# Kernel optimization log

Measured on AMD Instinct MI355X. Metric: run time of the kernel, lower is better.

## Reference

```python
import jax, jax.numpy as jnp
import numpy as np
from jax.scipy.special import logsumexp

B, DK, N, M = 16, 512, 1024, 1024
SINKHORN_ITERS = 5
EPS = 1e-8


def setup_inputs() -> dict:
    key = jax.random.key(0)
    k1, k2, k3, k4, k5 = jax.random.split(key, 5)
    return {
        "src_embedding": jax.random.normal(k1, (B, DK, N), dtype=jnp.float32),
        "tgt_embedding": jax.random.normal(k2, (B, DK, M), dtype=jnp.float32),
        "src": jax.random.normal(k3, (B, 3, N), dtype=jnp.float32),
        "tgt": jax.random.normal(k4, (B, 3, M), dtype=jnp.float32),
        # temperature must be positive; uniform in [0.05, 1.0)
        "temperature": jax.random.uniform(k5, (B,), dtype=jnp.float32, minval=0.05, maxval=1.0),
    }


def sinkhorn(scores, n_iters):
    # ZeroPad2d((0,1,0,1)): pad one slack row and one slack column with zeros
    scores = jnp.pad(scores, ((0, 0), (0, 1), (0, 1)))
    for _ in range(n_iters):
        # row normalization (all rows except slack row)
        top = scores[:, :-1, :] - logsumexp(scores[:, :-1, :], axis=2, keepdims=True)
        scores = jnp.concatenate([top, scores[:, -1:, :]], axis=1)
        # column normalization (all cols except slack col)
        left = scores[:, :, :-1] - logsumexp(scores[:, :, :-1], axis=1, keepdims=True)
        scores = jnp.concatenate([left, scores[:, :, -1:]], axis=2)
    return scores[:, :-1, :-1]


def reference(src_embedding, tgt_embedding, src, tgt, temperature):
    b, d_k, n = src_embedding.shape
    # [B, N, M] similarity scores
    dists = jnp.einsum('bdn,bdm->bnm', src_embedding, tgt_embedding) / jnp.sqrt(jnp.float32(d_k))
    affinity = dists / temperature[:, None, None]
    log_perm = sinkhorn(affinity, SINKHORN_ITERS)
    perm = jnp.exp(log_perm)                                             # [B,N,M]
    perm_norm = perm / (jnp.sum(perm, axis=2, keepdims=True) + EPS)      # [B,N,M]
    # soft correspondence: weighted_tgt[b,:,i] = sum_j perm_norm[b,i,j] * tgt[b,:,j]
    weighted_tgt = jnp.einsum('bdm,bnm->bdn', tgt, perm_norm)            # [B,3,N]
    weights = jnp.sum(perm, axis=-1, keepdims=True)                      # [B,N,1]
    weights_norm = weights / (jnp.sum(weights, axis=1, keepdims=True) + EPS)
    weights_norm = jnp.swapaxes(weights_norm, 1, 2)                      # [B,1,N]
    src_centroid = jnp.sum(src * weights_norm, axis=2, keepdims=True)    # [B,3,1]
    tgt_centroid = jnp.sum(weighted_tgt * weights_norm, axis=2, keepdims=True)
    src_centered = src - src_centroid
    corr_centered = (weighted_tgt - tgt_centroid) * weights_norm
    # weighted cross-covariance, batched 3x3
    H = jnp.einsum('bin,bjn->bij', src_centered, corr_centered)          # [B,3,3]
    # batched Procrustes via SVD (torch.svd: H = u diag(s) v^T; jnp: H = u diag(s) vh)
    u, s, vh = jnp.linalg.svd(H)
    v = jnp.swapaxes(vh, 1, 2)
    ut = jnp.swapaxes(u, 1, 2)
    r = jnp.matmul(v, ut)
    r_det = jnp.linalg.det(r)                                            # [B]
    diag = jnp.stack([jnp.ones_like(r_det), jnp.ones_like(r_det), r_det], axis=-1)  # [B,3]
    R = jnp.matmul(v * diag[:, None, :], ut)                             # [B,3,3]
    t = (jnp.matmul(-R, src_centroid) + tgt_centroid).reshape(b, 3)
    return R, t, perm_norm
```

## Files before the change

### kernel.cpp

```cpp
#include <hip/hip_runtime.h>
#include <math.h>

#define BB 16
#define NN 1024
#define MM 1024
#define DKK 512
#define RBLK 16
#define NRB  (NN/RBLK)

typedef short short8 __attribute__((ext_vector_type(8)));
typedef float f32x4 __attribute__((ext_vector_type(4)));

__device__ float g_u[BB*NN];
__device__ float g_v[BB*MM];
__device__ float g_w[BB*NN];
__device__ float g_wt[BB*3*NN];
__device__ float g_pm[BB*NRB*MM];
__device__ float g_ps[BB*NRB*MM];
__device__ __attribute__((aligned(16))) unsigned short gAh[BB*NN*DKK];
__device__ __attribute__((aligned(16))) unsigned short gAl[BB*NN*DKK];
__device__ __attribute__((aligned(16))) unsigned short gBh[BB*MM*DKK];
__device__ __attribute__((aligned(16))) unsigned short gBl[BB*MM*DKK];

__global__ __launch_bounds__(256) void zero_v_kernel() {
    int i = blockIdx.x*256 + threadIdx.x;
    if (i < BB*MM) g_v[i] = 0.0f;
}

__device__ __forceinline__ unsigned int bf16_rne(float x){
    unsigned int u = __float_as_uint(x);
    return (u + 0x7fffu + ((u>>16)&1u)) >> 16;
}

__device__ __forceinline__ void gl_lds(const void* g, void* l){
    __builtin_amdgcn_global_load_lds(
        (const __attribute__((address_space(1))) unsigned int*)g,
        (__attribute__((address_space(3))) unsigned int*)l, 16, 0, 0);
}

__global__ __launch_bounds__(256) void convert_split(const float* __restrict__ A,
                                                     const float* __restrict__ Bm) {
    int z = blockIdx.z;
    int which = z >> 4;
    int b = z & 15;
    const float* X = which ? Bm : A;
    unsigned short* Hh = which ? gBh : gAh;
    unsigned short* Hl = which ? gBl : gAl;
    int d0 = blockIdx.y * 64;
    int i0 = blockIdx.x * 64;
    __shared__ float T[64*65];
    const float* Xb = X + ((size_t)b*DKK + d0)*NN + i0;
    int t = threadIdx.x;
#pragma unroll
    for (int it=0; it<4; ++it){
        int lin = t + 256*it;
        int d = lin >> 4;
        int i4 = lin & 15;
        float4 v = *(const float4*)(Xb + (size_t)d*NN + i4*4);
        T[(i4*4+0)*65 + d] = v.x;
        T[(i4*4+1)*65 + d] = v.y;
        T[(i4*4+2)*65 + d] = v.z;
        T[(i4*4+3)*65 + d] = v.w;
    }
    __syncthreads();
    size_t obase = ((size_t)b*NN + i0)*DKK + d0;
#pragma unroll
    for (int it=0; it<2; ++it){
        int c = t + 256*it;
        int i = c >> 3;
        int p = c & 7;
        unsigned int hw[4], lw[4];
#pragma unroll
        for (int j=0;j<4;j++){
            float x0 = T[i*65 + p*8 + 2*j];
            float x1 = T[i*65 + p*8 + 2*j+1];
            unsigned int h0 = bf16_rne(x0);
            unsigned int h1 = bf16_rne(x1);
            float hf0 = __uint_as_float(h0<<16);
            float hf1 = __uint_as_float(h1<<16);
            unsigned int l0 = bf16_rne(x0 - hf0);
            unsigned int l1 = bf16_rne(x1 - hf1);
            hw[j] = h0 | (h1<<16);
            lw[j] = l0 | (l1<<16);
        }
        int pw = (p & 4) | ((p + (i>>1)) & 3);
        size_t eo = obase + (size_t)i*DKK + pw*8;
        uint4 hv; hv.x=hw[0]; hv.y=hw[1]; hv.z=hw[2]; hv.w=hw[3];
        uint4 lv; lv.x=lw[0]; lv.y=lw[1]; lv.z=lw[2]; lv.w=lw[3];
        *(uint4*)(Hh + eo) = hv;
        *(uint4*)(Hl + eo) = lv;
    }
}

__global__ __launch_bounds__(512,2) void gemm_mfma(const float* __restrict__ temp,
                                                   float* __restrict__ C) {
    int id   = blockIdx.x;
    int xcd  = id & 7;
    int slot = id >> 3;
    int b    = xcd*2 + (slot >> 4);
    int sub  = slot & 15;
    int i0   = (sub >> 2) << 8;
    int j0   = (sub & 3) << 8;
    __shared__ __attribute__((aligned(16))) char lds[131072];
    int t = threadIdx.x;
    int lane = t & 63, w = t >> 6;
    int wr = w >> 2, wc = w & 3;

    int rql = lane >> 2, cl = lane & 3;
    unsigned eoff = (unsigned)(b * (NN*DKK*2));
    unsigned offA = eoff + (unsigned)((i0 + w*32 + rql)*1024) + (unsigned)(cl*16);
    unsigned offB = eoff + (unsigned)((j0 + w*32 + rql)*1024) + (unsigned)(cl*16);
    int dq0 = w*2048;

    const char* pAh = (const char*)gAh;
    const char* pAl = (const char*)gAl;
    const char* pBh = (const char*)gBh;
    const char* pBl = (const char*)gBl;

    f32x4 acc[32];
#pragma unroll
    for (int q=0;q<32;q++) acc[q] = (f32x4){0.f,0.f,0.f,0.f};

    int fslot = ((lane>>4) + ((lane&15)>>1)) & 3;
    int faoff = (wr*128 + (lane&15))*64 + fslot*16;
    int fboff = (wc*64  + (lane&15))*64 + fslot*16;

    gl_lds(pAh + offA,          lds + 0      + dq0);
    gl_lds(pAh + offA + 16384,  lds + 0      + dq0 + 1024);
    gl_lds(pBh + offB,          lds + 65536  + dq0);
    gl_lds(pBh + offB + 16384,  lds + 65536  + dq0 + 1024);
    gl_lds(pAl + offA,          lds + 32768  + dq0);
    gl_lds(pAl + offA + 16384,  lds + 32768  + dq0 + 1024);
    gl_lds(pBl + offB,          lds + 98304  + dq0);
    gl_lds(pBl + offB + 16384,  lds + 98304  + dq0 + 1024);

    short8 ah[8], bh[4], al[8], bl[4];

    for (int ks=0; ks<16; ++ks){
        int par = (ks & 1) << 14;
        int nxt = 16384 - par;

        asm volatile("s_waitcnt vmcnt(4)" ::: "memory");
        __builtin_amdgcn_s_barrier();
        __builtin_amdgcn_sched_barrier(0);
        {
            const char* fa = lds + par + faoff;
            const char* fb = lds + 65536 + par + fboff;
#pragma unroll
            for (int mf=0;mf<8;mf++) ah[mf] = *(const short8*)(fa + mf*1024);
#pragma unroll
            for (int nf=0;nf<4;nf++) bh[nf] = *(const short8*)(fb + nf*1024);
        }
        if (ks < 15){
            offA += 64; offB += 64;
            gl_lds(pAh + offA,         lds + 0     + nxt + dq0);
            gl_lds(pAh + offA + 16384, lds + 0     + nxt + dq0 + 1024);
            gl_lds(pBh + offB,         lds + 65536 + nxt + dq0);
            gl_lds(pBh + offB + 16384, lds + 65536 + nxt + dq0 + 1024);
        }
        asm volatile("s_waitcnt lgkmcnt(0)" ::: "memory");
        __builtin_amdgcn_sched_barrier(0);
        __builtin_amdgcn_s_setprio(1);
#pragma unroll
        for (int nf=0;nf<4;nf++)
#pragma unroll
            for (int mf=0;mf<8;mf++)
                acc[mf*4+nf] = __builtin_amdgcn_mfma_f32_16x16x32_bf16(ah[mf], bh[nf], acc[mf*4+nf], 0,0,0);
        __builtin_amdgcn_s_setprio(0);
        __builtin_amdgcn_sched_barrier(0);

        if (ks < 15) asm volatile("s_waitcnt vmcnt(6)" ::: "memory");
        else         asm volatile("s_waitcnt vmcnt(2)" ::: "memory");
        __builtin_amdgcn_s_barrier();
        __builtin_amdgcn_sched_barrier(0);
        {
            const char* fa = lds + 32768 + par + faoff;
#pragma unroll
            for (int mf=0;mf<8;mf++) al[mf] = *(const short8*)(fa + mf*1024);
        }
        if (ks < 15){
            gl_lds(pAl + offA,         lds + 32768 + nxt + dq0);
            gl_lds(pAl + offA + 16384, lds + 32768 + nxt + dq0 + 1024);
        }
        asm volatile("s_waitcnt lgkmcnt(0)" ::: "memory");
        __builtin_amdgcn_sched_barrier(0);
        __builtin_amdgcn_s_setprio(1);
#pragma unroll
        for (int nf=0;nf<4;nf++)
#pragma unroll
            for (int mf=0;mf<8;mf++)
                acc[mf*4+nf] = __builtin_amdgcn_mfma_f32_16x16x32_bf16(al[mf], bh[nf], acc[mf*4+nf], 0,0,0);
        __builtin_amdgcn_s_setprio(0);
        __builtin_amdgcn_sched_barrier(0);

        if (ks < 15) asm volatile("s_waitcnt vmcnt(6)" ::: "memory");
        else         asm volatile("s_waitcnt vmcnt(0)" ::: "memory");
        __builtin_amdgcn_s_barrier();
        __builtin_amdgcn_sched_barrier(0);
        {
            const char* fb = lds + 98304 + par + fboff;
#pragma unroll
            for (int nf=0;nf<4;nf++) bl[nf] = *(const short8*)(fb + nf*1024);
        }
        if (ks < 15){
            gl_lds(pBl + offB,         lds + 98304 + nxt + dq0);
            gl_lds(pBl + offB + 16384, lds + 98304 + nxt + dq0 + 1024);
        }
        asm volatile("s_waitcnt lgkmcnt(0)" ::: "memory");
        __builtin_amdgcn_sched_barrier(0);
        __builtin_amdgcn_s_setprio(1);
#pragma unroll
        for (int nf=0;nf<4;nf++)
#pragma unroll
            for (int mf=0;mf<8;mf++)
                acc[mf*4+nf] = __builtin_amdgcn_mfma_f32_16x16x32_bf16(ah[mf], bl[nf], acc[mf*4+nf], 0,0,0);
        __builtin_amdgcn_s_setprio(0);
        __builtin_amdgcn_sched_barrier(0);
    }

    float scale = 1.0f/(22.62741699796952f * temp[b]);
    float* Cb = C + ((size_t)b<<20);
    int r0c = i0 + wr*128 + ((lane>>4)<<2);
    int c0c = j0 + wc*64 + (lane&15);
#pragma unroll
    for (int mf=0;mf<8;mf++){
#pragma unroll
        for (int r2=0;r2<4;r2++){
            float* rowp = Cb + (size_t)(r0c + mf*16 + r2)*MM + c0c;
#pragma unroll
            for (int nf=0;nf<4;nf++)
                rowp[nf*16] = acc[mf*4+nf][r2]*scale;
        }
    }
}

__global__ __launch_bounds__(256) void sink_iter(const float* __restrict__ S) {
    int b   = blockIdx.y;
    int rb  = blockIdx.x;
    int row0 = rb*RBLK;
    int t = threadIdx.x;
    __shared__ float Ls[RBLK*1028];
    __shared__ float v_l[1024];
    __shared__ float u_l[RBLK];

    float4 v4 = *(const float4*)(g_v + (b<<10) + t*4);
    *(float4*)(v_l + t*4) = v4;

    const float* Sb = S + ((size_t)b*NN + row0)*MM;
#pragma unroll
    for (int rr=0; rr<RBLK; ++rr){
        float4 s4 = *(const float4*)(Sb + (size_t)rr*MM + t*4);
        s4.x -= v4.x; s4.y -= v4.y; s4.z -= v4.z; s4.w -= v4.w;
        *(float4*)(&Ls[rr*1028 + t*4]) = s4;
    }
    __syncthreads();

    {
        int r = t >> 4, c = t & 15;
        const float* Lr = &Ls[r*1028 + c];
        float m = -INFINITY;
#pragma unroll
        for (int k=0;k<64;k++) m = fmaxf(m, Lr[16*k]);
#pragma unroll
        for (int off=1; off<16; off<<=1) m = fmaxf(m, __shfl_xor(m, off));
        m = fmaxf(m, 0.0f);
        float s = 0.0f;
#pragma unroll
        for (int k=0;k<64;k++) s += __expf(Lr[16*k] - m);
#pragma unroll
        for (int off=1; off<16; off<<=1) s += __shfl_xor(s, off);
        s += __expf(-m);
        float u = m + __logf(s);
        if (c==0){ u_l[r] = u; g_u[b*NN + row0 + r] = u; }
    }
    __syncthreads();

    float mm[4], ss[4];
#pragma unroll
    for (int q=0;q<4;q++){ mm[q]=-INFINITY; ss[q]=0.f; }
#pragma unroll
    for (int r=0;r<RBLK;++r){
        float ur = u_l[r];
        const float* Lr = &Ls[r*1028];
#pragma unroll
        for (int q=0;q<4;q++)
            mm[q] = fmaxf(mm[q], Lr[t + 256*q] - ur);
    }
#pragma unroll
    for (int r=0;r<RBLK;++r){
        float ur = u_l[r];
        const float* Lr = &Ls[r*1028];
#pragma unroll
        for (int q=0;q<4;q++)
            ss[q] += __expf(Lr[t + 256*q] - ur - mm[q]);
    }
    size_t pbase = ((size_t)(b*NRB + rb) << 10) + t;
#pragma unroll
    for (int q=0;q<4;q++){
        g_pm[pbase + 256*q] = mm[q] + v_l[t + 256*q];
        g_ps[pbase + 256*q] = ss[q];
    }
}

__global__ __launch_bounds__(256) void col_lse_combine() {
    int idx = blockIdx.x*256 + threadIdx.x;
    int b = idx >> 10; int j = idx & (MM-1);
    size_t base = ((size_t)(b*NRB) << 10) + j;
    float m[4], s[4];
#pragma unroll
    for (int k=0;k<4;k++){ m[k] = -INFINITY; s[k] = 0.0f; }
    for (int c=0;c<NRB;c+=4){
#pragma unroll
        for (int k=0;k<4;k++){
            float om = g_pm[base + ((size_t)(c+k)<<10)];
            float os = g_ps[base + ((size_t)(c+k)<<10)];
            float nm = fmaxf(m[k], om);
            s[k] = s[k]*__expf(m[k]-nm) + os*__expf(om-nm);
            m[k] = nm;
        }
    }
    float M01 = fmaxf(m[0], m[1]);
    float M23 = fmaxf(m[2], m[3]);
    float Mx  = fmaxf(M01, M23);
    float Sx  = s[0]*__expf(m[0]-Mx) + s[1]*__expf(m[1]-Mx)
              + s[2]*__expf(m[2]-Mx) + s[3]*__expf(m[3]-Mx);
    float nm = fmaxf(Mx, 0.0f);
    Sx = Sx*__expf(Mx-nm) + __expf(-nm);
    g_v[idx] = nm + __logf(Sx);
}

__global__ __launch_bounds__(256) void finalize_rows(float* __restrict__ S,
                                                     const float* __restrict__ tgt) {
    int row  = blockIdx.x*4 + (threadIdx.x>>6);
    int lane = threadIdx.x & 63;
    int b = row >> 10;
    int i = row & (NN-1);
    float ui = g_u[row];
    float4* srow = (float4*)(S + (size_t)row*MM);
    const float4* vb = (const float4*)(g_v + (b<<10));
    const float4* t0 = (const float4*)(tgt + (size_t)b*3*MM);
    const float4* t1 = (const float4*)(tgt + (size_t)b*3*MM + MM);
    const float4* t2 = (const float4*)(tgt + (size_t)b*3*MM + 2*MM);
    float p[16];
    float rs=0.f, a0=0.f, a1=0.f, a2=0.f;
#pragma unroll
    for (int k=0;k<4;k++){
        float4 s4 = srow[lane + 64*k];
        float4 v4 = vb[lane + 64*k];
        p[4*k+0] = __expf(s4.x - ui - v4.x);
        p[4*k+1] = __expf(s4.y - ui - v4.y);
        p[4*k+2] = __expf(s4.z - ui - v4.z);
        p[4*k+3] = __expf(s4.w - ui - v4.w);
        rs += p[4*k+0]+p[4*k+1]+p[4*k+2]+p[4*k+3];
        float4 w0 = t0[lane + 64*k];
        float4 w1 = t1[lane + 64*k];
        float4 w2 = t2[lane + 64*k];
        a0 += p[4*k+0]*w0.x + p[4*k+1]*w0.y + p[4*k+2]*w0.z + p[4*k+3]*w0.w;
        a1 += p[4*k+0]*w1.x + p[4*k+1]*w1.y + p[4*k+2]*w1.z + p[4*k+3]*w1.w;
        a2 += p[4*k+0]*w2.x + p[4*k+1]*w2.y + p[4*k+2]*w2.z + p[4*k+3]*w2.w;
    }
    for (int off=32; off; off>>=1){
        rs += __shfl_xor(rs, off);
        a0 += __shfl_xor(a0, off);
        a1 += __shfl_xor(a1, off);
        a2 += __shfl_xor(a2, off);
    }
    float inv = 1.0f/(rs + 1e-8f);
#pragma unroll
    for (int k=0;k<4;k++){
        srow[lane + 64*k] = make_float4(p[4*k+0]*inv, p[4*k+1]*inv, p[4*k+2]*inv, p[4*k+3]*inv);
    }
    if (lane==0){
        g_w[row] = rs;
        g_wt[(b*3+0)*NN + i] = a0*inv;
        g_wt[(b*3+1)*NN + i] = a1*inv;
        g_wt[(b*3+2)*NN + i] = a2*inv;
    }
}

__global__ __launch_bounds__(256) void procrustes(const float* __restrict__ src,
                                                  float* __restrict__ out) {
    int b = blockIdx.x;
    int t = threadIdx.x;
    __shared__ float red[256];
    auto bsum = [&](float v)->float{
        red[t]=v; __syncthreads();
        for (int o=128;o>0;o>>=1){ if(t<o) red[t]+=red[t+o]; __syncthreads(); }
        float r=red[0]; __syncthreads(); return r;
    };
    const float* wrow = g_w + b*NN;
    float pw=0.f;
    for (int i=t;i<NN;i+=256) pw += wrow[i];
    float W = bsum(pw);
    float winv = 1.0f/(W + 1e-8f);
    const float* sb  = src  + (size_t)b*3*NN;
    const float* wtb = g_wt + (size_t)b*3*NN;
    float sc[3], tc[3];
    for (int c=0;c<3;c++){
        float p1=0.f,p2=0.f;
        for (int i=t;i<NN;i+=256){
            float wn = wrow[i]*winv;
            p1 += sb[c*NN+i]*wn;
            p2 += wtb[c*NN+i]*wn;
        }
        sc[c]=bsum(p1);
        tc[c]=bsum(p2);
    }
    float H[9];
    for (int c=0;c<3;c++)
        for (int d=0;d<3;d++){
            float p=0.f;
            for (int i=t;i<NN;i+=256){
                float wn = wrow[i]*winv;
                p += (sb[c*NN+i]-sc[c]) * ((wtb[d*NN+i]-tc[d])*wn);
            }
            H[c*3+d]=bsum(p);
        }
    if (t==0){
        double Hd[3][3];
        for (int r2=0;r2<3;r2++) for (int c2=0;c2<3;c2++) Hd[r2][c2]=H[r2*3+c2];
        double K[3][3];
        for (int i2=0;i2<3;i2++)
            for (int j2=0;j2<3;j2++){
                double acc=0;
                for (int r2=0;r2<3;r2++) acc += Hd[r2][i2]*Hd[r2][j2];
                K[i2][j2]=acc;
            }
        double V[3][3]={{1,0,0},{0,1,0},{0,0,1}};
        const int PQ[3][2]={{0,1},{0,2},{1,2}};
        for (int sweep=0; sweep<30; ++sweep){
            double off = fabs(K[0][1])+fabs(K[0][2])+fabs(K[1][2]);
            if (off < 1e-26) break;
            for (int pi=0; pi<3; ++pi){
                int p = PQ[pi][0], q = PQ[pi][1];
                double apq = K[p][q];
                if (fabs(apq) < 1e-300) continue;
                double tau = (K[q][q]-K[p][p])/(2.0*apq);
                double tt  = (tau>=0.0?1.0:-1.0)/(fabs(tau)+sqrt(1.0+tau*tau));
                double c   = 1.0/sqrt(1.0+tt*tt);
                double s   = tt*c;
                double Kpp=K[p][p], Kqq=K[q][q];
                K[p][p] = Kpp - tt*apq;
                K[q][q] = Kqq + tt*apq;
                K[p][q] = 0.0; K[q][p] = 0.0;
                int r2 = 3-p-q;
                double Krp=K[r2][p], Krq=K[r2][q];
                K[r2][p] = c*Krp - s*Krq; K[p][r2]=K[r2][p];
                K[r2][q] = s*Krp + c*Krq; K[q][r2]=K[r2][q];
                for (int rr=0; rr<3; ++rr){
                    double vp=V[rr][p], vq=V[rr][q];
                    V[rr][p] = c*vp - s*vq;
                    V[rr][q] = s*vp + c*vq;
                }
            }
        }
        double lam[3]={K[0][0],K[1][1],K[2][2]};
        int o0=0,o1=1,o2=2,tmp;
        if (lam[o0]<lam[o1]){tmp=o0;o0=o1;o1=tmp;}
        if (lam[o0]<lam[o2]){tmp=o0;o0=o2;o2=tmp;}
        if (lam[o1]<lam[o2]){tmp=o1;o1=o2;o2=tmp;}
        int ord[3]={o0,o1,o2};
        double Vs[3][3], U[3][3];
        for (int k=0;k<3;k++)
            for (int r2=0;r2<3;r2++) Vs[r2][k]=V[r2][ord[k]];
        for (int k=0;k<3;k++){
            double ux = Hd[0][0]*Vs[0][k] + Hd[0][1]*Vs[1][k] + Hd[0][2]*Vs[2][k];
            double uy = Hd[1][0]*Vs[0][k] + Hd[1][1]*Vs[1][k] + Hd[1][2]*Vs[2][k];
            double uz = Hd[2][0]*Vs[0][k] + Hd[2][1]*Vs[1][k] + Hd[2][2]*Vs[2][k];
            double n = sqrt(ux*ux+uy*uy+uz*uz);
            if (n > 1e-30){ U[0][k]=ux/n; U[1][k]=uy/n; U[2][k]=uz/n; }
            else {
                double cx = U[1][0]*U[2][1]-U[2][0]*U[1][1];
                double cy = U[2][0]*U[0][1]-U[0][0]*U[2][1];
                double cz = U[0][0]*U[1][1]-U[1][0]*U[0][1];
                U[0][k]=cx; U[1][k]=cy; U[2][k]=cz;
            }
        }
        double rm[3][3];
        for (int i2=0;i2<3;i2++)
            for (int j2=0;j2<3;j2++)
                rm[i2][j2] = Vs[i2][0]*U[j2][0] + Vs[i2][1]*U[j2][1] + Vs[i2][2]*U[j2][2];
        double det = rm[0][0]*(rm[1][1]*rm[2][2]-rm[1][2]*rm[2][1])
                   - rm[0][1]*(rm[1][0]*rm[2][2]-rm[1][2]*rm[2][0])
                   + rm[0][2]*(rm[1][0]*rm[2][1]-rm[1][1]*rm[2][0]);
        double R[3][3];
        for (int i2=0;i2<3;i2++)
            for (int j2=0;j2<3;j2++)
                R[i2][j2] = Vs[i2][0]*U[j2][0] + Vs[i2][1]*U[j2][1] + det*Vs[i2][2]*U[j2][2];
        double tv[3];
        for (int i2=0;i2<3;i2++)
            tv[i2] = -(R[i2][0]*sc[0]+R[i2][1]*sc[1]+R[i2][2]*sc[2]) + tc[i2];
        for (int i2=0;i2<3;i2++)
            for (int j2=0;j2<3;j2++)
                out[b*9 + i2*3 + j2] = (float)R[i2][j2];
        for (int i2=0;i2<3;i2++)
            out[144 + b*3 + i2] = (float)tv[i2];
    }
}

extern "C" void kernel_launch(void* const* d_in, const int* in_sizes, int n_in,
                              void* d_out, int out_size, void* d_ws, size_t ws_size,
                              hipStream_t stream) {
    const float* src_emb = (const float*)d_in[0];
    const float* tgt_emb = (const float*)d_in[1];
    const float* src     = (const float*)d_in[2];
    const float* tgt     = (const float*)d_in[3];
    const float* temp    = (const float*)d_in[4];
    float* out = (float*)d_out;
    float* S = out + 192;

    hipLaunchKernelGGL(zero_v_kernel, dim3(64), dim3(256), 0, stream);
    hipLaunchKernelGGL(convert_split, dim3(16,8,32), dim3(256), 0, stream, src_emb, tgt_emb);
    hipLaunchKernelGGL(gemm_mfma, dim3(256), dim3(512), 0, stream, temp, S);
    for (int it=0; it<5; ++it){
        hipLaunchKernelGGL(sink_iter, dim3(NRB,BB), dim3(256), 0, stream, S);
        hipLaunchKernelGGL(col_lse_combine, dim3(64), dim3(256), 0, stream);
    }
    hipLaunchKernelGGL(finalize_rows, dim3(4096), dim3(256), 0, stream, S, tgt);
    hipLaunchKernelGGL(procrustes, dim3(16), dim3(256), 0, stream, src, out);
}
```

Before: 351.9 us.

## Merge GEMM pipeline stages, pad sinkhorn LDS, widen column combine, warp-shuffle procrustes

The bf16-split GEMM main loop now loads the Ah, Bh and Al fragments together behind one barrier and prefetches all of the next step's hi/lo A tiles at once. That drops one barrier and the explicit LDS wait stages per k-step. The sinkhorn row-tile LDS stride changes from 1028 to 1032 floats, which alters the bank mapping. The column log-sum-exp combine runs on 256 blocks of 64 threads with 8 independent accumulators and a tree merge, giving more parallelism and more memory-level parallelism. Procrustes loads its data once into registers and reduces with wave shuffles instead of repeated shared-memory tree reductions. The trade-offs are higher register pressure in the GEMM and a less staggered load/compute overlap.

```diff
diff --git a/kernel.cpp b/kernel.cpp
--- a/kernel.cpp
+++ b/kernel.cpp
@@ -7,6 +7,7 @@
 #define DKK 512
 #define RBLK 16
 #define NRB  (NN/RBLK)
+#define LSTR 1032
 
 typedef short short8 __attribute__((ext_vector_type(8)));
 typedef float f32x4 __attribute__((ext_vector_type(4)));
@@ -140,16 +141,19 @@
         int par = (ks & 1) << 14;
         int nxt = 16384 - par;
 
-        asm volatile("s_waitcnt vmcnt(4)" ::: "memory");
+        asm volatile("s_waitcnt vmcnt(2)" ::: "memory");
         __builtin_amdgcn_s_barrier();
         __builtin_amdgcn_sched_barrier(0);
         {
-            const char* fa = lds + par + faoff;
-            const char* fb = lds + 65536 + par + fboff;
+            const char* fa  = lds + par + faoff;
+            const char* fb  = lds + 65536 + par + fboff;
+            const char* fal = lds + 32768 + par + faoff;
 #pragma unroll
             for (int mf=0;mf<8;mf++) ah[mf] = *(const short8*)(fa + mf*1024);
 #pragma unroll
             for (int nf=0;nf<4;nf++) bh[nf] = *(const short8*)(fb + nf*1024);
+#pragma unroll
+            for (int mf=0;mf<8;mf++) al[mf] = *(const short8*)(fal + mf*1024);
         }
         if (ks < 15){
             offA += 64; offB += 64;
@@ -157,8 +161,9 @@
             gl_lds(pAh + offA + 16384, lds + 0     + nxt + dq0 + 1024);
             gl_lds(pBh + offB,         lds + 65536 + nxt + dq0);
             gl_lds(pBh + offB + 16384, lds + 65536 + nxt + dq0 + 1024);
-        }
-        asm volatile("s_waitcnt lgkmcnt(0)" ::: "memory");
+            gl_lds(pAl + offA,         lds + 32768 + nxt + dq0);
+            gl_lds(pAl + offA + 16384, lds + 32768 + nxt + dq0 + 1024);
+        }
         __builtin_amdgcn_sched_barrier(0);
         __builtin_amdgcn_s_setprio(1);
 #pragma unroll
@@ -166,25 +171,6 @@
 #pragma unroll
             for (int mf=0;mf<8;mf++)
                 acc[mf*4+nf] = __builtin_amdgcn_mfma_f32_16x16x32_bf16(ah[mf], bh[nf], acc[mf*4+nf], 0,0,0);
-        __builtin_amdgcn_s_setprio(0);
-        __builtin_amdgcn_sched_barrier(0);
-
-        if (ks < 15) asm volatile("s_waitcnt vmcnt(6)" ::: "memory");
-        else         asm volatile("s_waitcnt vmcnt(2)" ::: "memory");
-        __builtin_amdgcn_s_barrier();
-        __builtin_amdgcn_sched_barrier(0);
-        {
-            const char* fa = lds + 32768 + par + faoff;
-#pragma unroll
-            for (int mf=0;mf<8;mf++) al[mf] = *(const short8*)(fa + mf*1024);
-        }
-        if (ks < 15){
-            gl_lds(pAl + offA,         lds + 32768 + nxt + dq0);
-            gl_lds(pAl + offA + 16384, lds + 32768 + nxt + dq0 + 1024);
-        }
-        asm volatile("s_waitcnt lgkmcnt(0)" ::: "memory");
-        __builtin_amdgcn_sched_barrier(0);
-        __builtin_amdgcn_s_setprio(1);
 #pragma unroll
         for (int nf=0;nf<4;nf++)
 #pragma unroll
@@ -198,15 +184,14 @@
         __builtin_amdgcn_s_barrier();
         __builtin_amdgcn_sched_barrier(0);
         {
-            const char* fb = lds + 98304 + par + fboff;
-#pragma unroll
-            for (int nf=0;nf<4;nf++) bl[nf] = *(const short8*)(fb + nf*1024);
+            const char* fbl = lds + 98304 + par + fboff;
+#pragma unroll
+            for (int nf=0;nf<4;nf++) bl[nf] = *(const short8*)(fbl + nf*1024);
         }
         if (ks < 15){
             gl_lds(pBl + offB,         lds + 98304 + nxt + dq0);
             gl_lds(pBl + offB + 16384, lds + 98304 + nxt + dq0 + 1024);
         }
-        asm volatile("s_waitcnt lgkmcnt(0)" ::: "memory");
         __builtin_amdgcn_sched_barrier(0);
         __builtin_amdgcn_s_setprio(1);
 #pragma unroll
@@ -239,7 +224,7 @@
     int rb  = blockIdx.x;
     int row0 = rb*RBLK;
     int t = threadIdx.x;
-    __shared__ float Ls[RBLK*1028];
+    __shared__ float Ls[RBLK*LSTR];
     __shared__ float v_l[1024];
     __shared__ float u_l[RBLK];
 
@@ -251,13 +236,13 @@
     for (int rr=0; rr<RBLK; ++rr){
         float4 s4 = *(const float4*)(Sb + (size_t)rr*MM + t*4);
         s4.x -= v4.x; s4.y -= v4.y; s4.z -= v4.z; s4.w -= v4.w;
-        *(float4*)(&Ls[rr*1028 + t*4]) = s4;
+        *(float4*)(&Ls[rr*LSTR + t*4]) = s4;
     }
     __syncthreads();
 
     {
         int r = t >> 4, c = t & 15;
-        const float* Lr = &Ls[r*1028 + c];
+        const float* Lr = &Ls[r*LSTR + c];
         float m = -INFINITY;
 #pragma unroll
         for (int k=0;k<64;k++) m = fmaxf(m, Lr[16*k]);
@@ -281,7 +266,7 @@
 #pragma unroll
     for (int r=0;r<RBLK;++r){
         float ur = u_l[r];
-        const float* Lr = &Ls[r*1028];
+        const float* Lr = &Ls[r*LSTR];
 #pragma unroll
         for (int q=0;q<4;q++)
             mm[q] = fmaxf(mm[q], Lr[t + 256*q] - ur);
@@ -289,7 +274,7 @@
 #pragma unroll
     for (int r=0;r<RBLK;++r){
         float ur = u_l[r];
-        const float* Lr = &Ls[r*1028];
+        const float* Lr = &Ls[r*LSTR];
 #pragma unroll
         for (int q=0;q<4;q++)
             ss[q] += __expf(Lr[t + 256*q] - ur - mm[q]);
@@ -302,16 +287,16 @@
     }
 }
 
-__global__ __launch_bounds__(256) void col_lse_combine() {
-    int idx = blockIdx.x*256 + threadIdx.x;
+__global__ __launch_bounds__(64) void col_lse_combine() {
+    int idx = blockIdx.x*64 + threadIdx.x;
     int b = idx >> 10; int j = idx & (MM-1);
     size_t base = ((size_t)(b*NRB) << 10) + j;
-    float m[4], s[4];
-#pragma unroll
-    for (int k=0;k<4;k++){ m[k] = -INFINITY; s[k] = 0.0f; }
-    for (int c=0;c<NRB;c+=4){
-#pragma unroll
-        for (int k=0;k<4;k++){
+    float m[8], s[8];
+#pragma unroll
+    for (int k=0;k<8;k++){ m[k] = -INFINITY; s[k] = 0.0f; }
+    for (int c=0;c<NRB;c+=8){
+#pragma unroll
+        for (int k=0;k<8;k++){
             float om = g_pm[base + ((size_t)(c+k)<<10)];
             float os = g_ps[base + ((size_t)(c+k)<<10)];
             float nm = fmaxf(m[k], om);
@@ -319,13 +304,17 @@
             m[k] = nm;
         }
     }
-    float M01 = fmaxf(m[0], m[1]);
-    float M23 = fmaxf(m[2], m[3]);
-    float Mx  = fmaxf(M01, M23);
-    float Sx  = s[0]*__expf(m[0]-Mx) + s[1]*__expf(m[1]-Mx)
-              + s[2]*__expf(m[2]-Mx) + s[3]*__expf(m[3]-Mx);
-    float nm = fmaxf(Mx, 0.0f);
-    Sx = Sx*__expf(Mx-nm) + __expf(-nm);
+#pragma unroll
+    for (int st=1; st<8; st<<=1){
+#pragma unroll
+        for (int k=0;k<8;k+=2*st){
+            float nm = fmaxf(m[k], m[k+st]);
+            s[k] = s[k]*__expf(m[k]-nm) + s[k+st]*__expf(m[k+st]-nm);
+            m[k] = nm;
+        }
+    }
+    float nm = fmaxf(m[0], 0.0f);
+    float Sx = s[0]*__expf(m[0]-nm) + __expf(-nm);
     g_v[idx] = nm + __logf(Sx);
 }
 
@@ -382,40 +371,69 @@
                                                   float* __restrict__ out) {
     int b = blockIdx.x;
     int t = threadIdx.x;
-    __shared__ float red[256];
-    auto bsum = [&](float v)->float{
-        red[t]=v; __syncthreads();
-        for (int o=128;o>0;o>>=1){ if(t<o) red[t]+=red[t+o]; __syncthreads(); }
-        float r=red[0]; __syncthreads(); return r;
-    };
+    int lane = t & 63, w = t >> 6;
+    __shared__ float part[4][16];
     const float* wrow = g_w + b*NN;
-    float pw=0.f;
-    for (int i=t;i<NN;i+=256) pw += wrow[i];
-    float W = bsum(pw);
-    float winv = 1.0f/(W + 1e-8f);
     const float* sb  = src  + (size_t)b*3*NN;
     const float* wtb = g_wt + (size_t)b*3*NN;
-    float sc[3], tc[3];
+
+    float wv[4], sv[3][4], tv3[3][4];
+#pragma unroll
+    for (int k=0;k<4;k++){
+        int i = t + 256*k;
+        wv[k] = wrow[i];
+#pragma unroll
+        for (int c=0;c<3;c++){
+            sv[c][k]  = sb[c*NN+i];
+            tv3[c][k] = wtb[c*NN+i];
+        }
+    }
+
+    auto block_reduce = [&](float* v, int nv){
+        for (int jx=0;jx<nv;jx++){
+            float x = v[jx];
+            for (int off=32;off;off>>=1) x += __shfl_xor(x, off);
+            if (lane==0) part[w][jx] = x;
+        }
+        __syncthreads();
+        for (int jx=0;jx<nv;jx++)
+            v[jx] = part[0][jx]+part[1][jx]+part[2][jx]+part[3][jx];
+        __syncthreads();
+    };
+
+    float W = wv[0]+wv[1]+wv[2]+wv[3];
+    block_reduce(&W, 1);
+    float winv = 1.0f/(W + 1e-8f);
+    float wn[4];
+#pragma unroll
+    for (int k=0;k<4;k++) wn[k] = wv[k]*winv;
+
+    float a[6];
+#pragma unroll
     for (int c=0;c<3;c++){
         float p1=0.f,p2=0.f;
-        for (int i=t;i<NN;i+=256){
-            float wn = wrow[i]*winv;
-            p1 += sb[c*NN+i]*wn;
-            p2 += wtb[c*NN+i]*wn;
-        }
-        sc[c]=bsum(p1);
-        tc[c]=bsum(p2);
-    }
+#pragma unroll
+        for (int k=0;k<4;k++){ p1 += sv[c][k]*wn[k]; p2 += tv3[c][k]*wn[k]; }
+        a[c]=p1; a[3+c]=p2;
+    }
+    block_reduce(a, 6);
+    float sc[3], tc[3];
+#pragma unroll
+    for (int c=0;c<3;c++){ sc[c]=a[c]; tc[c]=a[3+c]; }
+
     float H[9];
+#pragma unroll
     for (int c=0;c<3;c++)
+#pragma unroll
         for (int d=0;d<3;d++){
             float p=0.f;
-            for (int i=t;i<NN;i+=256){
-                float wn = wrow[i]*winv;
-                p += (sb[c*NN+i]-sc[c]) * ((wtb[d*NN+i]-tc[d])*wn);
-            }
-            H[c*3+d]=bsum(p);
-        }
+#pragma unroll
+            for (int k=0;k<4;k++)
+                p += (sv[c][k]-sc[c]) * ((tv3[d][k]-tc[d])*wn[k]);
+            H[c*3+d]=p;
+        }
+    block_reduce(H, 9);
+
     if (t==0){
         double Hd[3][3];
         for (int r2=0;r2<3;r2++) for (int c2=0;c2<3;c2++) Hd[r2][c2]=H[r2*3+c2];
@@ -487,14 +505,14 @@
         for (int i2=0;i2<3;i2++)
             for (int j2=0;j2<3;j2++)
                 R[i2][j2] = Vs[i2][0]*U[j2][0] + Vs[i2][1]*U[j2][1] + det*Vs[i2][2]*U[j2][2];
-        double tv[3];
+        double tvv[3];
         for (int i2=0;i2<3;i2++)
-            tv[i2] = -(R[i2][0]*sc[0]+R[i2][1]*sc[1]+R[i2][2]*sc[2]) + tc[i2];
+            tvv[i2] = -(R[i2][0]*sc[0]+R[i2][1]*sc[1]+R[i2][2]*sc[2]) + tc[i2];
         for (int i2=0;i2<3;i2++)
             for (int j2=0;j2<3;j2++)
                 out[b*9 + i2*3 + j2] = (float)R[i2][j2];
         for (int i2=0;i2<3;i2++)
-            out[144 + b*3 + i2] = (float)tv[i2];
+            out[144 + b*3 + i2] = (float)tvv[i2];
     }
 }
 
@@ -514,7 +532,7 @@
     hipLaunchKernelGGL(gemm_mfma, dim3(256), dim3(512), 0, stream, temp, S);
     for (int it=0; it<5; ++it){
         hipLaunchKernelGGL(sink_iter, dim3(NRB,BB), dim3(256), 0, stream, S);
-        hipLaunchKernelGGL(col_lse_combine, dim3(64), dim3(256), 0, stream);
+        hipLaunchKernelGGL(col_lse_combine, dim3(256), dim3(64), 0, stream);
     }
     hipLaunchKernelGGL(finalize_rows, dim3(4096), dim3(256), 0, stream, S, tgt);
     hipLaunchKernelGGL(procrustes, dim3(16), dim3(256), 0, stream, src, out);
```

After: 336.0 us. -4.5%, faster.
